# Optimization experiments

Hardware: AMD Instinct MI355X
Metric: run time of the kernel (lower is better)

## Reference

```python
import jax, jax.numpy as jnp
import numpy as np

SCALE_FACTORS = (1, 2, 4)
N, T, F = 4096, 128, 128
MARKET = 64
MIX = sum(T // k for k in SCALE_FACTORS)  # 224


def hardswish(x):
    return x * jnp.clip(x + 3.0, 0.0, 6.0) * (1.0 / 6.0)


def layernorm2d(x, g, b, eps=1e-5):
    # LayerNorm with normalized_shape == last two dims (as in torch nn.LayerNorm((A, B)))
    mu = jnp.mean(x, axis=(-2, -1), keepdims=True)
    var = jnp.var(x, axis=(-2, -1), keepdims=True)
    return (x - mu) * jax.lax.rsqrt(var + eps) * g + b


def setup_inputs() -> dict:
    key = jax.random.key(0)
    ks = jax.random.split(key, 32)
    inp = {"x": jax.random.normal(ks[0], (N, T, F), jnp.float32)}
    i = 1
    for si, k in enumerate(SCALE_FACTORS):
        tk = T // k
        inp[f"cw{si}"] = jax.random.normal(ks[i], (F, F, k), jnp.float32) * 0.05; i += 1
        inp[f"cb{si}"] = jnp.zeros((F,), jnp.float32)
        inp[f"lg{si}"] = jnp.ones((tk, F), jnp.float32)
        inp[f"lb{si}"] = jnp.zeros((tk, F), jnp.float32)
        inp[f"L1_{si}"] = jax.random.normal(ks[i], (tk, tk), jnp.float32) * 0.01; i += 1
        inp[f"L2_{si}"] = jax.random.normal(ks[i], (tk, tk), jnp.float32) * 0.01; i += 1
    inp["fc_w"] = jax.random.normal(ks[i], (1, F), jnp.float32) * 0.05; i += 1
    inp["fc_b"] = jnp.zeros((1,), jnp.float32)
    inp["sm_lg"] = jnp.ones((N, MIX), jnp.float32)
    inp["sm_lb"] = jnp.zeros((N, MIX), jnp.float32)
    inp["M1"] = jax.random.normal(ks[i], (MARKET, N), jnp.float32); i += 1
    inp["M2"] = jax.random.normal(ks[i], (N, MARKET), jnp.float32); i += 1
    inp["sm_fc_w"] = jax.random.normal(ks[i], (1, 2 * MIX), jnp.float32) * 0.02; i += 1
    inp["sm_fc_b"] = jnp.zeros((1,), jnp.float32)
    return inp


def _forward(x, cw0, cb0, lg0, lb0, L1_0, L2_0,
             cw1, cb1, lg1, lb1, L1_1, L2_1,
             cw2, cb2, lg2, lb2, L1_2, L2_2,
             fc_w, fc_b, sm_lg, sm_lb, M1, M2, sm_fc_w, sm_fc_b):
    n, t, f = x.shape
    per_scale = ((cw0, cb0, lg0, lb0, L1_0, L2_0),
                 (cw1, cb1, lg1, lb1, L1_1, L2_1),
                 (cw2, cb2, lg2, lb2, L1_2, L2_2))
    parts = []
    for k, (cw, cb, lg, lb, L1, L2) in zip(SCALE_FACTORS, per_scale):
        tk = t // k
        # Conv1d(kernel=k, stride=k) == blockwise contraction over non-overlapping windows
        xr = x.transpose(0, 2, 1).reshape(n, f, tk, k)          # (n, F_in, tk, k)
        xt = jnp.einsum('nitk,oik->nto', xr, cw) + cb            # (n, tk, F)
        # TimeMixing: ragged prefix loop == single lower-triangular matmul over time
        mask = jnp.tril(jnp.ones((tk, tk), x.dtype))
        h = layernorm2d(xt, lg, lb)
        u = hardswish(jnp.einsum('ts,nsf->ntf', L1 * mask, h))
        v = jnp.einsum('ts,nsf->ntf', L2 * mask, u)
        xt = xt + v
        parts.append(xt @ fc_w[0] + fc_b[0])                     # (n, tk)
    h = jnp.concatenate(parts, axis=1)                           # (n, MIX)
    # StockMixing
    hn = layernorm2d(h, sm_lg, sm_lb)
    z = M2 @ hardswish(M1 @ hn)                                  # (n, MIX)
    out = jnp.concatenate([h, h + z], axis=1)                    # (n, 2*MIX)
    return out @ sm_fc_w[0][:, None] + sm_fc_b                   # (n, 1)


def reference(x, cw0, cb0, lg0, lb0, L1_0, L2_0,
              cw1, cb1, lg1, lb1, L1_1, L2_1,
              cw2, cb2, lg2, lb2, L1_2, L2_2,
              fc_w, fc_b, sm_lg, sm_lb, M1, M2, sm_fc_w, sm_fc_b):
    return _forward(x, cw0, cb0, lg0, lb0, L1_0, L2_0,
                    cw1, cb1, lg1, lb1, L1_1, L2_1,
                    cw2, cb2, lg2, lb2, L1_2, L2_2,
                    fc_w, fc_b, sm_lg, sm_lb, M1, M2, sm_fc_w, sm_fc_b)
```

## Files before the change

### kernel.cpp

```cpp
#include <hip/hip_runtime.h>
#include <stdint.h>

typedef __attribute__((ext_vector_type(8))) short short8;
typedef __attribute__((ext_vector_type(4))) float f32x4;
typedef __attribute__((ext_vector_type(4))) unsigned short us4;

__device__ __forceinline__ unsigned short f2bf(float f) {
  union { float f; unsigned int i; } v; v.f = f;
  unsigned int r = (v.i + 0x7FFFu + ((v.i >> 16) & 1u)) >> 16;
  return (unsigned short)r;
}
__device__ __forceinline__ float hswish(float x) {
  float t = fminf(fmaxf(x + 3.f, 0.f), 6.f);
  return x * t * (1.f / 6.f);
}

__device__ __forceinline__ void cwprep(const float* __restrict__ cw,
                                       unsigned short* __restrict__ dst,
                                       int rel, int k, int NKS) {
  int e = rel & 7;
  int lane = (rel >> 3) & 63;
  int rest = rel >> 9;
  int ksl = rest % NKS, ot = rest / NKS;
  int m = ksl * 32 + (lane >> 4) * 8 + e;
  int o = ot * 16 + (lane & 15);
  int j = m >> 7, i = m & 127;
  dst[rel] = f2bf(cw[(o * 128 + i) * k + j]);
}

__global__ void prep_kernel(const float* __restrict__ cw0,
                            const float* __restrict__ cw1,
                            const float* __restrict__ cw2,
                            unsigned short* __restrict__ cwP0,
                            unsigned short* __restrict__ cwP1,
                            unsigned short* __restrict__ cwP2) {
  int idx = blockIdx.x * 256 + threadIdx.x;
  if (idx < 16384)       cwprep(cw0, cwP0, idx,          1,  4);
  else if (idx < 49152)  cwprep(cw1, cwP1, idx - 16384,  2,  8);
  else if (idx < 114688) cwprep(cw2, cwP2, idx - 49152,  4, 16);
}

__device__ __forceinline__ short8 lfrag(const float* __restrict__ L, int TK,
                                        int srow, int scol) {
  const float4 v0 = *(const float4*)(L + srow * TK + scol);
  const float4 v1 = *(const float4*)(L + srow * TK + scol + 4);
  short8 r;
  r[0] = (scol     <= srow) ? (short)f2bf(v0.x) : (short)0;
  r[1] = (scol + 1 <= srow) ? (short)f2bf(v0.y) : (short)0;
  r[2] = (scol + 2 <= srow) ? (short)f2bf(v0.z) : (short)0;
  r[3] = (scol + 3 <= srow) ? (short)f2bf(v0.w) : (short)0;
  r[4] = (scol + 4 <= srow) ? (short)f2bf(v1.x) : (short)0;
  r[5] = (scol + 5 <= srow) ? (short)f2bf(v1.y) : (short)0;
  r[6] = (scol + 6 <= srow) ? (short)f2bf(v1.z) : (short)0;
  r[7] = (scol + 7 <= srow) ? (short)f2bf(v1.w) : (short)0;
  return r;
}

template <int S, int nTT>
__device__ __forceinline__ void conv_o(const unsigned short* __restrict__ xb,
                                       const unsigned short* __restrict__ cwP,
                                       f32x4 (&acc)[nTT][2],
                                       int wave, int lane, int quad, int l16) {
  constexpr int NKS = (128 << S) / 32;
#pragma unroll
  for (int tt = 0; tt < nTT; ++tt)
#pragma unroll
    for (int oo = 0; oo < 2; ++oo)
      acc[tt][oo] = (f32x4){0.f, 0.f, 0.f, 0.f};

#pragma unroll
  for (int ks = 0; ks < NKS; ++ks) {
    const int m = ks * 32 + quad * 8;
    short8 a[nTT];
#pragma unroll
    for (int tt = 0; tt < nTT; ++tt) {
      int t = tt * 16 + l16;
      a[tt] = *(const short8*)&xb[((t << S) + (m >> 7)) * 136 + (m & 127)];
    }
#pragma unroll
    for (int oo = 0; oo < 2; ++oo) {
      const short8 b = *(const short8*)&cwP[(((wave * 2 + oo) * NKS + ks) * 64 + lane) * 8];
#pragma unroll
      for (int tt = 0; tt < nTT; ++tt)
        acc[tt][oo] = __builtin_amdgcn_mfma_f32_16x16x32_bf16(a[tt], b, acc[tt][oo], 0, 0, 0);
    }
  }
}

template <int S, int nTT>
__device__ __forceinline__ void post_o(unsigned short* __restrict__ HT,
                                       float* __restrict__ scratch,
                                       f32x4 (&acc)[nTT][2],
                                       const float* __restrict__ cb,
                                       const float* __restrict__ lg,
                                       const float* __restrict__ lb,
                                       const float* __restrict__ L1,
                                       const float* __restrict__ L2,
                                       int tid, int wave, int lane,
                                       int quad, int l16) {
  constexpr int TK    = 128 >> S;
  constexpr int OFF   = (S == 0) ? 0 : (S == 1 ? 128 : 192);
  constexpr int NTS   = TK / 32;
  constexpr int HTP   = TK + 8;
  constexpr int nTOwn = (S == 0) ? 2 : 1;
  constexpr int nFF   = (S == 2) ? 4 : 8;
  const int ffBase  = (S == 2) ? ((wave >> 1) * 4) : 0;
  const int maxTown = (S == 0) ? (wave + 4) : ((S == 1) ? wave : (wave & 1));

  float sum = 0.f, ss = 0.f;
#pragma unroll
  for (int oo = 0; oo < 2; ++oo) {
    float cbv = cb[(wave * 2 + oo) * 16 + l16];
#pragma unroll
    for (int tt = 0; tt < nTT; ++tt)
#pragma unroll
      for (int r = 0; r < 4; ++r) {
        float v = acc[tt][oo][r] + cbv;
        acc[tt][oo][r] = v;
        sum += v; ss += v * v;
      }
  }
#pragma unroll
  for (int m = 32; m >= 1; m >>= 1) {
    sum += __shfl_xor(sum, m);
    ss  += __shfl_xor(ss, m);
  }
  if (lane == 0) { scratch[352 + wave * 2] = sum; scratch[353 + wave * 2] = ss; }

#pragma unroll
  for (int tt = 0; tt < nTT; ++tt)
#pragma unroll
    for (int r = 0; r < 4; ++r) {
      float v = acc[tt][0][r] * scratch[(wave * 2) * 16 + l16]
              + acc[tt][1][r] * scratch[(wave * 2 + 1) * 16 + l16];
      v += __shfl_xor(v, 1); v += __shfl_xor(v, 2);
      v += __shfl_xor(v, 4); v += __shfl_xor(v, 8);
      if (l16 == 0)
        atomicAdd(&scratch[128 + OFF + tt * 16 + quad * 4 + r], v);
    }
  __syncthreads();

  const float Sm = scratch[352] + scratch[354] + scratch[356] + scratch[358];
  const float Sq = scratch[353] + scratch[355] + scratch[357] + scratch[359];
  const float mu = Sm * (1.f / (float)(TK * 128));
  const float rsig = rsqrtf(Sq * (1.f / (float)(TK * 128)) - mu * mu + 1e-5f);

#pragma unroll
  for (int oo = 0; oo < 2; ++oo) {
    const int o = (wave * 2 + oo) * 16 + l16;
#pragma unroll
    for (int tt = 0; tt < nTT; ++tt)
#pragma unroll
      for (int r = 0; r < 4; ++r) {
        const int t = tt * 16 + quad * 4 + r;
        float hv = (acc[tt][oo][r] - mu) * rsig * lg[t * 128 + o] + lb[t * 128 + o];
        HT[o * HTP + t] = f2bf(hv);
      }
  }
  __syncthreads();

  f32x4 uacc[nTOwn][nFF];
#pragma unroll
  for (int tt = 0; tt < nTOwn; ++tt)
#pragma unroll
    for (int ff = 0; ff < nFF; ++ff)
      uacc[tt][ff] = (f32x4){0.f, 0.f, 0.f, 0.f};

#pragma unroll
  for (int ks = 0; ks < NTS; ++ks) {
    const int k0 = ks * 32;
    if (k0 <= maxTown * 16 + 15) {
      short8 a[nTOwn];
#pragma unroll
      for (int tt = 0; tt < nTOwn; ++tt) {
        const int tw = (S == 0) ? (wave + tt * 4) : maxTown;
        if (k0 <= tw * 16 + 15)
          a[tt] = lfrag(L1, TK, tw * 16 + l16, k0 + quad * 8);
      }
#pragma unroll
      for (int ff = 0; ff < nFF; ++ff) {
        const short8 b = *(const short8*)&HT[((ffBase + ff) * 16 + l16) * HTP + k0 + quad * 8];
#pragma unroll
        for (int tt = 0; tt < nTOwn; ++tt) {
          const int tw = (S == 0) ? (wave + tt * 4) : maxTown;
          if (k0 <= tw * 16 + 15)
            uacc[tt][ff] = __builtin_amdgcn_mfma_f32_16x16x32_bf16(a[tt], b, uacc[tt][ff], 0, 0, 0);
        }
      }
    }
  }
  __syncthreads();

#pragma unroll
  for (int tt = 0; tt < nTOwn; ++tt) {
    const int tw = (S == 0) ? (wave + tt * 4) : maxTown;
#pragma unroll
    for (int ff = 0; ff < nFF; ++ff) {
      const int f = (ffBase + ff) * 16 + l16;
#pragma unroll
      for (int r = 0; r < 4; ++r) {
        const int t = tw * 16 + quad * 4 + r;
        HT[f * HTP + t] = f2bf(hswish(uacc[tt][ff][r]));
      }
    }
  }
  __syncthreads();

#pragma unroll
  for (int tt = 0; tt < nTOwn; ++tt)
#pragma unroll
    for (int ff = 0; ff < nFF; ++ff)
      uacc[tt][ff] = (f32x4){0.f, 0.f, 0.f, 0.f};

#pragma unroll
  for (int ks = 0; ks < NTS; ++ks) {
    const int k0 = ks * 32;
    if (k0 <= maxTown * 16 + 15) {
      short8 a[nTOwn];
#pragma unroll
      for (int tt = 0; tt < nTOwn; ++tt) {
        const int tw = (S == 0) ? (wave + tt * 4) : maxTown;
        if (k0 <= tw * 16 + 15)
          a[tt] = lfrag(L2, TK, tw * 16 + l16, k0 + quad * 8);
      }
#pragma unroll
      for (int ff = 0; ff < nFF; ++ff) {
        const short8 b = *(const short8*)&HT[((ffBase + ff) * 16 + l16) * HTP + k0 + quad * 8];
#pragma unroll
        for (int tt = 0; tt < nTOwn; ++tt) {
          const int tw = (S == 0) ? (wave + tt * 4) : maxTown;
          if (k0 <= tw * 16 + 15)
            uacc[tt][ff] = __builtin_amdgcn_mfma_f32_16x16x32_bf16(a[tt], b, uacc[tt][ff], 0, 0, 0);
        }
      }
    }
  }

#pragma unroll
  for (int tt = 0; tt < nTOwn; ++tt) {
    const int tw = (S == 0) ? (wave + tt * 4) : maxTown;
#pragma unroll
    for (int r = 0; r < 4; ++r) {
      float v = 0.f;
#pragma unroll
      for (int ff = 0; ff < nFF; ++ff)
        v += uacc[tt][ff][r] * scratch[(ffBase + ff) * 16 + l16];
      v += __shfl_xor(v, 1); v += __shfl_xor(v, 2);
      v += __shfl_xor(v, 4); v += __shfl_xor(v, 8);
      if (l16 == 0)
        atomicAdd(&scratch[128 + OFF + tw * 16 + quad * 4 + r], v);
    }
  }
}

__launch_bounds__(256, 2)
__global__ void s1_fused(const float* __restrict__ x,
                         const float* __restrict__ cb0, const float* __restrict__ lg0,
                         const float* __restrict__ lb0, const float* __restrict__ L1_0,
                         const float* __restrict__ L2_0,
                         const float* __restrict__ cb1, const float* __restrict__ lg1,
                         const float* __restrict__ lb1, const float* __restrict__ L1_1,
                         const float* __restrict__ L2_1,
                         const float* __restrict__ cb2, const float* __restrict__ lg2,
                         const float* __restrict__ lb2, const float* __restrict__ L1_2,
                         const float* __restrict__ L2_2,
                         const float* __restrict__ fc_w, const float* __restrict__ fc_b,
                         const unsigned short* __restrict__ cwP0,
                         const unsigned short* __restrict__ cwP1,
                         const unsigned short* __restrict__ cwP2,
                         float* __restrict__ h_out,
                         float* __restrict__ stats) {
  extern __shared__ char smem[];
  unsigned short* xb = (unsigned short*)smem;
  float* scratch = (float*)(smem + 34816);

  const int tid  = threadIdx.x;
  const int wave = tid >> 6;
  const int lane = tid & 63;
  const int quad = lane >> 4;
  const int l16  = lane & 15;
  const int n    = blockIdx.x;
  const float* xn = x + (size_t)n * 16384;

  if (tid < 128) scratch[tid] = fc_w[tid];
  if (tid < 224) scratch[128 + tid] = 0.f;

  for (int i = tid; i < 4096; i += 256) {
    int t = i >> 5, c4 = (i & 31) * 4;
    const float4 v = *(const float4*)(xn + t * 128 + c4);
    us4 p; p[0] = f2bf(v.x); p[1] = f2bf(v.y); p[2] = f2bf(v.z); p[3] = f2bf(v.w);
    *(us4*)&xb[t * 136 + c4] = p;
  }
  __syncthreads();

  f32x4 acc0[8][2], acc1[4][2], acc2[2][2];
  conv_o<0, 8>(xb, cwP0, acc0, wave, lane, quad, l16);
  conv_o<1, 4>(xb, cwP1, acc1, wave, lane, quad, l16);
  conv_o<2, 2>(xb, cwP2, acc2, wave, lane, quad, l16);

  unsigned short* HT = xb;
  post_o<2, 2>(HT, scratch, acc2, cb2, lg2, lb2, L1_2, L2_2, tid, wave, lane, quad, l16);
  post_o<1, 4>(HT, scratch, acc1, cb1, lg1, lb1, L1_1, L2_1, tid, wave, lane, quad, l16);
  post_o<0, 8>(HT, scratch, acc0, cb0, lg0, lb0, L1_0, L2_0, tid, wave, lane, quad, l16);

  __syncthreads();

  float hv = 0.f;
  if (tid < 224) {
    hv = scratch[128 + tid] + fc_b[0];
    h_out[(size_t)n * 224 + tid] = hv;
  }
  float s = hv, sq = hv * hv;
#pragma unroll
  for (int m = 32; m >= 1; m >>= 1) {
    s  += __shfl_xor(s, m);
    sq += __shfl_xor(sq, m);
  }
  __syncthreads();
  if (lane == 0) { scratch[352 + wave * 2] = s; scratch[353 + wave * 2] = sq; }
  __syncthreads();
  if (tid == 0) {
    atomicAdd(&stats[0], scratch[352] + scratch[354] + scratch[356] + scratch[358]);
    atomicAdd(&stats[1], scratch[353] + scratch[355] + scratch[357] + scratch[359]);
  }
}

__global__ void mix1_kernel(const float* __restrict__ h,
                            const float* __restrict__ sm_lg,
                            const float* __restrict__ sm_lb,
                            const float* __restrict__ M1,
                            const float* __restrict__ stats,
                            float* __restrict__ A) {
  const int m = blockIdx.x;
  const int seg = blockIdx.y;
  const int r = threadIdx.x & 63;
  const int ch = threadIdx.x >> 6;
  const float inv = 1.f / 917504.f;
  float mu = stats[0] * inv;
  float var = stats[1] * inv - mu * mu;
  float rsig = rsqrtf(var + 1e-5f);
  float a0 = 0.f, a1 = 0.f, a2 = 0.f, a3 = 0.f;
  int n0 = seg * 1024 + ch * 256;
  for (int i = 0; i < 256; i += 4) {
    int n = n0 + i;
    float h0 = (h[(n    ) * 224 + m] - mu) * rsig * sm_lg[(n    ) * 224 + m] + sm_lb[(n    ) * 224 + m];
    float h1 = (h[(n + 1) * 224 + m] - mu) * rsig * sm_lg[(n + 1) * 224 + m] + sm_lb[(n + 1) * 224 + m];
    float h2 = (h[(n + 2) * 224 + m] - mu) * rsig * sm_lg[(n + 2) * 224 + m] + sm_lb[(n + 2) * 224 + m];
    float h3 = (h[(n + 3) * 224 + m] - mu) * rsig * sm_lg[(n + 3) * 224 + m] + sm_lb[(n + 3) * 224 + m];
    a0 += M1[r * 4096 + n    ] * h0;
    a1 += M1[r * 4096 + n + 1] * h1;
    a2 += M1[r * 4096 + n + 2] * h2;
    a3 += M1[r * 4096 + n + 3] * h3;
  }
  __shared__ float red[256];
  red[threadIdx.x] = (a0 + a1) + (a2 + a3);
  __syncthreads();
  if (threadIdx.x < 64)
    atomicAdd(&A[threadIdx.x * 224 + m],
              red[threadIdx.x] + red[64 + threadIdx.x] + red[128 + threadIdx.x] + red[192 + threadIdx.x]);
}

__global__ void out_kernel(const float* __restrict__ h,
                           const float* __restrict__ A,
                           const float* __restrict__ M2,
                           const float* __restrict__ sm_fc_w,
                           const float* __restrict__ sm_fc_b,
                           float* __restrict__ out) {
  const int tid = threadIdx.x;
  const int wave = tid >> 6, lane = tid & 63;
  __shared__ float red[256];
  __shared__ float cv[64];

  {
    const int r = tid & 63, ch = tid >> 6;
    float acc = 0.f;
    for (int j = ch; j < 224; j += 4)
      acc += hswish(A[r * 224 + j]) * sm_fc_w[224 + j];
    red[tid] = acc;
  }
  __syncthreads();
  if (tid < 64)
    cv[tid] = red[tid] + red[64 + tid] + red[128 + tid] + red[192 + tid];
  __syncthreads();

  const int n = blockIdx.x * 4 + wave;
  float acc = M2[n * 64 + lane] * cv[lane];
  for (int j = lane; j < 224; j += 64)
    acc += h[n * 224 + j] * (sm_fc_w[j] + sm_fc_w[224 + j]);
#pragma unroll
  for (int m = 32; m >= 1; m >>= 1) acc += __shfl_xor(acc, m);
  if (lane == 0) out[n] = acc + sm_fc_b[0];
}

extern "C" void kernel_launch(void* const* d_in, const int* in_sizes, int n_in,
                              void* d_out, int out_size, void* d_ws, size_t ws_size,
                              hipStream_t stream) {
  const float* x      = (const float*)d_in[0];
  const float* cw0    = (const float*)d_in[1];
  const float* cb0    = (const float*)d_in[2];
  const float* lg0    = (const float*)d_in[3];
  const float* lb0    = (const float*)d_in[4];
  const float* L1_0   = (const float*)d_in[5];
  const float* L2_0   = (const float*)d_in[6];
  const float* cw1    = (const float*)d_in[7];
  const float* cb1    = (const float*)d_in[8];
  const float* lg1    = (const float*)d_in[9];
  const float* lb1    = (const float*)d_in[10];
  const float* L1_1   = (const float*)d_in[11];
  const float* L2_1   = (const float*)d_in[12];
  const float* cw2    = (const float*)d_in[13];
  const float* cb2    = (const float*)d_in[14];
  const float* lg2    = (const float*)d_in[15];
  const float* lb2    = (const float*)d_in[16];
  const float* L1_2   = (const float*)d_in[17];
  const float* L2_2   = (const float*)d_in[18];
  const float* fc_w   = (const float*)d_in[19];
  const float* fc_b   = (const float*)d_in[20];
  const float* sm_lg  = (const float*)d_in[21];
  const float* sm_lb  = (const float*)d_in[22];
  const float* M1     = (const float*)d_in[23];
  const float* M2     = (const float*)d_in[24];
  const float* sm_fc_w = (const float*)d_in[25];
  const float* sm_fc_b = (const float*)d_in[26];

  char* ws = (char*)d_ws;
  unsigned short* cwP0 = (unsigned short*)(ws);
  unsigned short* cwP1 = (unsigned short*)(ws + 32768);
  unsigned short* cwP2 = (unsigned short*)(ws + 98304);
  float* h     = (float*)(ws + 229376);
  float* stats = (float*)(ws + 3899392);
  float* A     = (float*)(ws + 3899648);

  prep_kernel<<<448, 256, 0, stream>>>(cw0, cw1, cw2, cwP0, cwP1, cwP2);

  hipMemsetAsync(ws + 3899392, 0, 57600, stream);

  constexpr size_t S1_LDS = 34816 + 362 * 4;

  s1_fused<<<4096, 256, S1_LDS, stream>>>(
      x,
      cb0, lg0, lb0, L1_0, L2_0,
      cb1, lg1, lb1, L1_1, L2_1,
      cb2, lg2, lb2, L1_2, L2_2,
      fc_w, fc_b, cwP0, cwP1, cwP2, h, stats);

  mix1_kernel<<<dim3(224, 4), 256, 0, stream>>>(h, sm_lg, sm_lb, M1, stats, A);
  out_kernel<<<1024, 256, 0, stream>>>(h, A, M2, sm_fc_w, sm_fc_b, (float*)d_out);
}
```

Baseline: 844.3 us.

## Split fused per-scale kernel, prepack masked L tiles, transpose M1 for mixing

Splits the single fused kernel that handled all three time scales into three per-scale kernel launches. Each launch keeps fewer accumulators live and gets a higher launch-bounds occupancy target, at the cost of reading x three times. The prep kernel also pre-converts the masked L1/L2 matrices into bf16 MFMA fragment layout, so the post-processing loads one short8 instead of converting on the fly. It also writes M1 transposed, giving mix1 coalesced access, and packs LDS stores into 4-wide vectors. The fast path only runs when the workspace is large enough; otherwise it falls back to on-the-fly conversion.

New measurement: 953.1 us. 12.9% more time.

```diff
diff --git a/kernel.cpp b/kernel.cpp
--- a/kernel.cpp
+++ b/kernel.cpp
@@ -28,16 +28,45 @@
   dst[rel] = f2bf(cw[(o * 128 + i) * k + j]);
 }
 
+__device__ __forceinline__ void lbprep(const float* __restrict__ L,
+                                       unsigned short* __restrict__ dst,
+                                       int rel, int TK) {
+  int NTS = TK / 32;
+  int e = rel & 7;
+  int lane = (rel >> 3) & 63;
+  int rest = rel >> 9;
+  int ks = rest % NTS, tt = rest / NTS;
+  int trow = tt * 16 + (lane & 15);
+  int col = ks * 32 + (lane >> 4) * 8 + e;
+  dst[rel] = (col <= trow) ? f2bf(L[trow * TK + col]) : (unsigned short)0;
+}
+
 __global__ void prep_kernel(const float* __restrict__ cw0,
                             const float* __restrict__ cw1,
                             const float* __restrict__ cw2,
+                            const float* __restrict__ L1_0, const float* __restrict__ L2_0,
+                            const float* __restrict__ L1_1, const float* __restrict__ L2_1,
+                            const float* __restrict__ L1_2, const float* __restrict__ L2_2,
+                            const float* __restrict__ M1,
                             unsigned short* __restrict__ cwP0,
                             unsigned short* __restrict__ cwP1,
-                            unsigned short* __restrict__ cwP2) {
+                            unsigned short* __restrict__ cwP2,
+                            unsigned short* __restrict__ Lb,
+                            float* __restrict__ M1T) {
   int idx = blockIdx.x * 256 + threadIdx.x;
-  if (idx < 16384)       cwprep(cw0, cwP0, idx,          1,  4);
-  else if (idx < 49152)  cwprep(cw1, cwP1, idx - 16384,  2,  8);
-  else if (idx < 114688) cwprep(cw2, cwP2, idx - 49152,  4, 16);
+  if (idx < 16384)       { cwprep(cw0, cwP0, idx,          1,  4); return; }
+  if (idx < 49152)       { cwprep(cw1, cwP1, idx - 16384,  2,  8); return; }
+  if (idx < 114688)      { cwprep(cw2, cwP2, idx - 49152,  4, 16); return; }
+  if (Lb == nullptr) return;
+  int rel = idx - 114688;
+  if (rel < 16384)       { lbprep(L1_0, Lb,          rel,          128); return; }
+  if (rel < 32768)       { lbprep(L2_0, Lb + 16384,  rel - 16384,  128); return; }
+  if (rel < 36864)       { lbprep(L1_1, Lb + 32768,  rel - 32768,   64); return; }
+  if (rel < 40960)       { lbprep(L2_1, Lb + 36864,  rel - 36864,   64); return; }
+  if (rel < 41984)       { lbprep(L1_2, Lb + 40960,  rel - 40960,   32); return; }
+  if (rel < 43008)       { lbprep(L2_2, Lb + 41984,  rel - 41984,   32); return; }
+  int t = rel - 43008;
+  if (t < 262144) M1T[t] = M1[(t & 63) * 4096 + (t >> 6)];
 }
 
 __device__ __forceinline__ short8 lfrag(const float* __restrict__ L, int TK,
@@ -87,7 +116,7 @@
   }
 }
 
-template <int S, int nTT>
+template <int S, int nTT, bool PK>
 __device__ __forceinline__ void post_o(unsigned short* __restrict__ HT,
                                        float* __restrict__ scratch,
                                        f32x4 (&acc)[nTT][2],
@@ -96,6 +125,8 @@
                                        const float* __restrict__ lb,
                                        const float* __restrict__ L1,
                                        const float* __restrict__ L2,
+                                       const unsigned short* __restrict__ L1p,
+                                       const unsigned short* __restrict__ L2p,
                                        int tid, int wave, int lane,
                                        int quad, int l16) {
   constexpr int TK    = 128 >> S;
@@ -149,13 +180,15 @@
   for (int oo = 0; oo < 2; ++oo) {
     const int o = (wave * 2 + oo) * 16 + l16;
 #pragma unroll
-    for (int tt = 0; tt < nTT; ++tt)
+    for (int tt = 0; tt < nTT; ++tt) {
+      us4 p;
 #pragma unroll
       for (int r = 0; r < 4; ++r) {
         const int t = tt * 16 + quad * 4 + r;
-        float hv = (acc[tt][oo][r] - mu) * rsig * lg[t * 128 + o] + lb[t * 128 + o];
-        HT[o * HTP + t] = f2bf(hv);
+        p[r] = f2bf((acc[tt][oo][r] - mu) * rsig * lg[t * 128 + o] + lb[t * 128 + o]);
       }
+      *(us4*)&HT[o * HTP + tt * 16 + quad * 4] = p;
+    }
   }
   __syncthreads();
 
@@ -174,8 +207,12 @@
 #pragma unroll
       for (int tt = 0; tt < nTOwn; ++tt) {
         const int tw = (S == 0) ? (wave + tt * 4) : maxTown;
-        if (k0 <= tw * 16 + 15)
-          a[tt] = lfrag(L1, TK, tw * 16 + l16, k0 + quad * 8);
+        if (k0 <= tw * 16 + 15) {
+          if constexpr (PK)
+            a[tt] = *(const short8*)&L1p[((tw * NTS + ks) * 64 + lane) * 8];
+          else
+            a[tt] = lfrag(L1, TK, tw * 16 + l16, k0 + quad * 8);
+        }
       }
 #pragma unroll
       for (int ff = 0; ff < nFF; ++ff) {
@@ -197,11 +234,11 @@
 #pragma unroll
     for (int ff = 0; ff < nFF; ++ff) {
       const int f = (ffBase + ff) * 16 + l16;
-#pragma unroll
-      for (int r = 0; r < 4; ++r) {
-        const int t = tw * 16 + quad * 4 + r;
-        HT[f * HTP + t] = f2bf(hswish(uacc[tt][ff][r]));
-      }
+      us4 p;
+#pragma unroll
+      for (int r = 0; r < 4; ++r)
+        p[r] = f2bf(hswish(uacc[tt][ff][r]));
+      *(us4*)&HT[f * HTP + tw * 16 + quad * 4] = p;
     }
   }
   __syncthreads();
@@ -220,8 +257,12 @@
 #pragma unroll
       for (int tt = 0; tt < nTOwn; ++tt) {
         const int tw = (S == 0) ? (wave + tt * 4) : maxTown;
-        if (k0 <= tw * 16 + 15)
-          a[tt] = lfrag(L2, TK, tw * 16 + l16, k0 + quad * 8);
+        if (k0 <= tw * 16 + 15) {
+          if constexpr (PK)
+            a[tt] = *(const short8*)&L2p[((tw * NTS + ks) * 64 + lane) * 8];
+          else
+            a[tt] = lfrag(L2, TK, tw * 16 + l16, k0 + quad * 8);
+        }
       }
 #pragma unroll
       for (int ff = 0; ff < nFF; ++ff) {
@@ -253,23 +294,22 @@
   }
 }
 
-__launch_bounds__(256, 2)
-__global__ void s1_fused(const float* __restrict__ x,
-                         const float* __restrict__ cb0, const float* __restrict__ lg0,
-                         const float* __restrict__ lb0, const float* __restrict__ L1_0,
-                         const float* __restrict__ L2_0,
-                         const float* __restrict__ cb1, const float* __restrict__ lg1,
-                         const float* __restrict__ lb1, const float* __restrict__ L1_1,
-                         const float* __restrict__ L2_1,
-                         const float* __restrict__ cb2, const float* __restrict__ lg2,
-                         const float* __restrict__ lb2, const float* __restrict__ L1_2,
-                         const float* __restrict__ L2_2,
-                         const float* __restrict__ fc_w, const float* __restrict__ fc_b,
-                         const unsigned short* __restrict__ cwP0,
-                         const unsigned short* __restrict__ cwP1,
-                         const unsigned short* __restrict__ cwP2,
-                         float* __restrict__ h_out,
-                         float* __restrict__ stats) {
+template <int S, bool PK>
+__launch_bounds__(256, (S == 0) ? 3 : 4)
+__global__ void s1s(const float* __restrict__ x,
+                    const float* __restrict__ cb, const float* __restrict__ lg,
+                    const float* __restrict__ lb,
+                    const float* __restrict__ L1, const float* __restrict__ L2,
+                    const unsigned short* __restrict__ L1p,
+                    const unsigned short* __restrict__ L2p,
+                    const float* __restrict__ fc_w, const float* __restrict__ fc_b,
+                    const unsigned short* __restrict__ cwP,
+                    float* __restrict__ h_out,
+                    float* __restrict__ stats) {
+  constexpr int TK  = 128 >> S;
+  constexpr int OFF = (S == 0) ? 0 : (S == 1 ? 128 : 192);
+  constexpr int nTT = 8 >> S;
+
   extern __shared__ char smem[];
   unsigned short* xb = (unsigned short*)smem;
   float* scratch = (float*)(smem + 34816);
@@ -283,7 +323,7 @@
   const float* xn = x + (size_t)n * 16384;
 
   if (tid < 128) scratch[tid] = fc_w[tid];
-  if (tid < 224) scratch[128 + tid] = 0.f;
+  if (tid < TK) scratch[128 + OFF + tid] = 0.f;
 
   for (int i = tid; i < 4096; i += 256) {
     int t = i >> 5, c4 = (i & 31) * 4;
@@ -293,22 +333,19 @@
   }
   __syncthreads();
 
-  f32x4 acc0[8][2], acc1[4][2], acc2[2][2];
-  conv_o<0, 8>(xb, cwP0, acc0, wave, lane, quad, l16);
-  conv_o<1, 4>(xb, cwP1, acc1, wave, lane, quad, l16);
-  conv_o<2, 2>(xb, cwP2, acc2, wave, lane, quad, l16);
+  f32x4 acc[nTT][2];
+  conv_o<S, nTT>(xb, cwP, acc, wave, lane, quad, l16);
 
   unsigned short* HT = xb;
-  post_o<2, 2>(HT, scratch, acc2, cb2, lg2, lb2, L1_2, L2_2, tid, wave, lane, quad, l16);
-  post_o<1, 4>(HT, scratch, acc1, cb1, lg1, lb1, L1_1, L2_1, tid, wave, lane, quad, l16);
-  post_o<0, 8>(HT, scratch, acc0, cb0, lg0, lb0, L1_0, L2_0, tid, wave, lane, quad, l16);
+  post_o<S, nTT, PK>(HT, scratch, acc, cb, lg, lb, L1, L2, L1p, L2p,
+                     tid, wave, lane, quad, l16);
 
   __syncthreads();
 
   float hv = 0.f;
-  if (tid < 224) {
-    hv = scratch[128 + tid] + fc_b[0];
-    h_out[(size_t)n * 224 + tid] = hv;
+  if (tid < TK) {
+    hv = scratch[128 + OFF + tid] + fc_b[0];
+    h_out[(size_t)n * 224 + OFF + tid] = hv;
   }
   float s = hv, sq = hv * hv;
 #pragma unroll
@@ -325,6 +362,7 @@
   }
 }
 
+template <bool TR>
 __global__ void mix1_kernel(const float* __restrict__ h,
                             const float* __restrict__ sm_lg,
                             const float* __restrict__ sm_lb,
@@ -347,16 +385,23 @@
     float h1 = (h[(n + 1) * 224 + m] - mu) * rsig * sm_lg[(n + 1) * 224 + m] + sm_lb[(n + 1) * 224 + m];
     float h2 = (h[(n + 2) * 224 + m] - mu) * rsig * sm_lg[(n + 2) * 224 + m] + sm_lb[(n + 2) * 224 + m];
     float h3 = (h[(n + 3) * 224 + m] - mu) * rsig * sm_lg[(n + 3) * 224 + m] + sm_lb[(n + 3) * 224 + m];
-    a0 += M1[r * 4096 + n    ] * h0;
-    a1 += M1[r * 4096 + n + 1] * h1;
-    a2 += M1[r * 4096 + n + 2] * h2;
-    a3 += M1[r * 4096 + n + 3] * h3;
+    if (TR) {
+      a0 += M1[(n    ) * 64 + r] * h0;
+      a1 += M1[(n + 1) * 64 + r] * h1;
+      a2 += M1[(n + 2) * 64 + r] * h2;
+      a3 += M1[(n + 3) * 64 + r] * h3;
+    } else {
+      a0 += M1[r * 4096 + n    ] * h0;
+      a1 += M1[r * 4096 + n + 1] * h1;
+      a2 += M1[r * 4096 + n + 2] * h2;
+      a3 += M1[r * 4096 + n + 3] * h3;
+    }
   }
   __shared__ float red[256];
   red[threadIdx.x] = (a0 + a1) + (a2 + a3);
   __syncthreads();
   if (threadIdx.x < 64)
-    atomicAdd(&A[threadIdx.x * 224 + m],
+    atomicAdd(&A[m * 64 + threadIdx.x],
               red[threadIdx.x] + red[64 + threadIdx.x] + red[128 + threadIdx.x] + red[192 + threadIdx.x]);
 }
 
@@ -375,7 +420,7 @@
     const int r = tid & 63, ch = tid >> 6;
     float acc = 0.f;
     for (int j = ch; j < 224; j += 4)
-      acc += hswish(A[r * 224 + j]) * sm_fc_w[224 + j];
+      acc += hswish(A[j * 64 + r]) * sm_fc_w[224 + j];
     red[tid] = acc;
   }
   __syncthreads();
@@ -430,20 +475,35 @@
   float* h     = (float*)(ws + 229376);
   float* stats = (float*)(ws + 3899392);
   float* A     = (float*)(ws + 3899648);
-
-  prep_kernel<<<448, 256, 0, stream>>>(cw0, cw1, cw2, cwP0, cwP1, cwP2);
+  const bool extra = ws_size >= 5091840;
+  unsigned short* Lb = extra ? (unsigned short*)(ws + 3957248) : nullptr;
+  float* M1T         = extra ? (float*)(ws + 4043264) : nullptr;
+
+  prep_kernel<<<1640, 256, 0, stream>>>(cw0, cw1, cw2,
+                                        L1_0, L2_0, L1_1, L2_1, L1_2, L2_2, M1,
+                                        cwP0, cwP1, cwP2, Lb, M1T);
 
   hipMemsetAsync(ws + 3899392, 0, 57600, stream);
 
   constexpr size_t S1_LDS = 34816 + 362 * 4;
 
-  s1_fused<<<4096, 256, S1_LDS, stream>>>(
-      x,
-      cb0, lg0, lb0, L1_0, L2_0,
-      cb1, lg1, lb1, L1_1, L2_1,
-      cb2, lg2, lb2, L1_2, L2_2,
-      fc_w, fc_b, cwP0, cwP1, cwP2, h, stats);
-
-  mix1_kernel<<<dim3(224, 4), 256, 0, stream>>>(h, sm_lg, sm_lb, M1, stats, A);
+  if (extra) {
+    s1s<0, true><<<4096, 256, S1_LDS, stream>>>(x, cb0, lg0, lb0, L1_0, L2_0,
+        Lb, Lb + 16384, fc_w, fc_b, cwP0, h, stats);
+    s1s<1, true><<<4096, 256, S1_LDS, stream>>>(x, cb1, lg1, lb1, L1_1, L2_1,
+        Lb + 32768, Lb + 36864, fc_w, fc_b, cwP1, h, stats);
+    s1s<2, true><<<4096, 256, S1_LDS, stream>>>(x, cb2, lg2, lb2, L1_2, L2_2,
+        Lb + 40960, Lb + 41984, fc_w, fc_b, cwP2, h, stats);
+    mix1_kernel<true><<<dim3(224, 4), 256, 0, stream>>>(h, sm_lg, sm_lb, M1T, stats, A);
+  } else {
+    s1s<0, false><<<4096, 256, S1_LDS, stream>>>(x, cb0, lg0, lb0, L1_0, L2_0,
+        nullptr, nullptr, fc_w, fc_b, cwP0, h, stats);
+    s1s<1, false><<<4096, 256, S1_LDS, stream>>>(x, cb1, lg1, lb1, L1_1, L2_1,
+        nullptr, nullptr, fc_w, fc_b, cwP1, h, stats);
+    s1s<2, false><<<4096, 256, S1_LDS, stream>>>(x, cb2, lg2, lb2, L1_2, L2_2,
+        nullptr, nullptr, fc_w, fc_b, cwP2, h, stats);
+    mix1_kernel<false><<<dim3(224, 4), 256, 0, stream>>>(h, sm_lg, sm_lb, M1, stats, A);
+  }
+
   out_kernel<<<1024, 256, 0, stream>>>(h, A, M2, sm_fc_w, sm_fc_b, (float*)d_out);
 }
```
